# Optimization experiments

Measured on AMD Instinct MI355X. Metric: run time of the kernel, lower is better.

Reference implementation:

```python
import jax, jax.numpy as jnp
import numpy as np

B, S, HID = 1, 2048, 2048
NH = 16
QL, KVL = 1536, 512
DN, DR, DV = 128, 64, 128
DQ = DN + DR  # 192
IH, ID = 4, 128
TOPK = 1024
EPS = 1e-6
THETA = 10000.0


def rope_interleaved(x, cos, sin):
    # x: (b,s,h,d); cos/sin: (s,d//2); pairs are (x[...,2i], x[...,2i+1])
    xr = x[..., 0::2]
    xi = x[..., 1::2]
    c = cos[None, :, None, :]
    s = sin[None, :, None, :]
    yr = xr * c - xi * s
    yi = xr * s + xi * c
    return jnp.stack([yr, yi], axis=-1).reshape(x.shape)


def rope_noninterleaved(x, cos, sin):
    # rotate-half style: pairs are (x[...,i], x[...,i+d/2])
    d = x.shape[-1] // 2
    x1, x2 = x[..., :d], x[..., d:]
    c = cos[None, :, None, :]
    s = sin[None, :, None, :]
    return jnp.concatenate([x1 * c - x2 * s, x1 * s + x2 * c], axis=-1)


def rmsnorm(x, w):
    var = jnp.mean(x * x, axis=-1, keepdims=True)
    return w * (x * jax.lax.rsqrt(var + EPS))


def layernorm(x, g, b):
    mu = jnp.mean(x, axis=-1, keepdims=True)
    var = jnp.mean((x - mu) ** 2, axis=-1, keepdims=True)
    return (x - mu) * jax.lax.rsqrt(var + EPS) * g + b


def setup_inputs() -> dict:
    key = jax.random.key(0)
    ks = jax.random.split(key, 12)
    std = 0.02
    x = jax.random.normal(ks[0], (B, S, HID), jnp.float32)
    pos = jnp.arange(S, dtype=jnp.float32)
    inv_freq = THETA ** (-jnp.arange(0, DR, 2, dtype=jnp.float32) / DR)
    ang = pos[:, None] * inv_freq[None, :]  # (S, DR//2)
    cos, sin = jnp.cos(ang), jnp.sin(ang)
    mask = jnp.where(jnp.tril(jnp.ones((S, S), bool)), 0.0, -1e9).astype(jnp.float32)
    return {
        "x": x, "cos": cos, "sin": sin, "mask": mask,
        "Wq_a": jax.random.normal(ks[1], (HID, QL), jnp.float32) * std,
        "q_norm_w": jnp.ones((QL,), jnp.float32),
        "Wq_b": jax.random.normal(ks[2], (QL, NH * DQ), jnp.float32) * std,
        "Wkv_a": jax.random.normal(ks[3], (HID, KVL + DR), jnp.float32) * std,
        "kv_norm_w": jnp.ones((KVL,), jnp.float32),
        "Wkv_b": jax.random.normal(ks[4], (KVL, NH * (DN + DV)), jnp.float32) * std,
        "Wo": jax.random.normal(ks[5], (NH * DV, HID), jnp.float32) * std,
        "IWq_b": jax.random.normal(ks[6], (QL, IH * ID), jnp.float32) * std,
        "IWk": jax.random.normal(ks[7], (HID, ID), jnp.float32) * std,
        "Ik_norm_w": jnp.ones((ID,), jnp.float32),
        "Ik_norm_b": jnp.zeros((ID,), jnp.float32),
        "IWproj": jax.random.normal(ks[8], (HID, IH), jnp.float32) * std,
    }


def indexer(x, qr, cos, sin, mask, IWq_b, IWk, Ik_norm_w, Ik_norm_b, IWproj):
    b, s, _ = x.shape
    q = (qr @ IWq_b).reshape(b, s, IH, ID)
    q_pe, q_nope = q[..., :DR], q[..., DR:]
    q_pe = rope_noninterleaved(q_pe, cos, sin)
    q = jnp.concatenate([q_pe, q_nope], axis=-1)
    k = layernorm(x @ IWk, Ik_norm_w, Ik_norm_b)  # (b,s,ID)
    k_pe = rope_noninterleaved(k[:, :, None, :DR], cos, sin)[:, :, 0]
    k = jnp.concatenate([k_pe, k[..., DR:]], axis=-1)
    weights = (x @ IWproj) * (IH ** -0.5) * (ID ** -0.5)  # (b,s,IH)
    logits = jax.nn.relu(jnp.einsum('bthd,bsd->btsh', q, k))
    index_score = jnp.einsum('btsh,bth->bts', logits, weights)
    index_score = index_score + mask[None]
    k_top = min(TOPK, s)
    topk_idx = jax.lax.top_k(index_score, k_top)[1]  # (b,s,k)
    bi = jnp.arange(b)[:, None, None]
    si = jnp.arange(s)[None, :, None]
    index_mask = jnp.full((b, s, s), -1e9, jnp.float32).at[bi, si, topk_idx].set(0.0)
    return index_mask


def reference(x, cos, sin, mask, Wq_a, q_norm_w, Wq_b, Wkv_a, kv_norm_w, Wkv_b, Wo,
              IWq_b, IWk, Ik_norm_w, Ik_norm_b, IWproj):
    b, s, _ = x.shape
    qr = rmsnorm(x @ Wq_a, q_norm_w)  # (b,s,QL)
    q = (qr @ Wq_b).reshape(b, s, NH, DQ)
    q_nope, q_pe = q[..., :DN], q[..., DN:]
    q_pe = rope_interleaved(q_pe, cos, sin)
    q = jnp.concatenate([q_nope, q_pe], axis=-1)
    kv_full = x @ Wkv_a
    kv, k_pe = kv_full[..., :KVL], kv_full[..., KVL:]
    kv = rmsnorm(kv, kv_norm_w)
    k_pe = rope_interleaved(k_pe[:, :, None, :], cos, sin)  # (b,s,1,DR)
    kv_exp = (kv @ Wkv_b).reshape(b, s, NH, DN + DV)
    k_nope, v = kv_exp[..., :DN], kv_exp[..., DN:]
    k = jnp.concatenate([k_nope, jnp.broadcast_to(k_pe, (b, s, NH, DR))], axis=-1)
    scores = jnp.einsum('bshd,bthd->bsht', q, k) * (DQ ** -0.5)
    index_mask = indexer(x, qr, cos, sin, mask, IWq_b, IWk, Ik_norm_w, Ik_norm_b, IWproj)
    scores = scores + index_mask[:, :, None, :] + mask[None, :, None, :]
    probs = jax.nn.softmax(scores, axis=-1)
    out = jnp.einsum('bsht,bthd->bshd', probs, v).reshape(b, s, NH * DV)
    return out @ Wo
```

## Files before the change

kernel.cpp:

```cpp
#include <hip/hip_runtime.h>
#include <math.h>
#include <stdint.h>

#define S 2048
#define HID 2048
#define NH 16
#define QL 1536
#define KVL 512
#define DN 128
#define DR 64
#define DV 128
#define DQ 192
#define IH 4
#define ID 128
#define TOPK 1024

#define N1 2244
#define N2 3584

#define CDIV(a,b) (((a)+(b)-1)/(b))

typedef float f32x4 __attribute__((ext_vector_type(4)));
typedef short bf16x8 __attribute__((ext_vector_type(8)));

__device__ __forceinline__ ushort f2b(float f) {
    uint32_t u = __float_as_uint(f);
    u += 0x7fffu + ((u >> 16) & 1u);
    return (ushort)(u >> 16);
}

#define GLL16(g, l)                                                            \
    __builtin_amdgcn_global_load_lds(                                          \
        (const __attribute__((address_space(1))) void*)(g),                    \
        (__attribute__((address_space(3))) void*)(l), 16, 0, 0)

__global__ __launch_bounds__(256) void gemm_bt(const ushort* __restrict__ A,
                                               const ushort* __restrict__ BT,
                                               float* __restrict__ C,
                                               int M, int N, int K) {
    __shared__ ushort As[2][128 * 64];
    __shared__ ushort Bs[2][128 * 64];
    const int tid = threadIdx.x;
    const int w = tid >> 6, l = tid & 63;
    const int quad = l >> 4, lane = l & 15;
    const int row0 = blockIdx.y * 128, col0 = blockIdx.x * 128;
    const int wr = (w >> 1) * 64, wc = (w & 1) * 64;
    f32x4 acc[4][4];
#pragma unroll
    for (int i = 0; i < 4; i++)
#pragma unroll
        for (int j = 0; j < 4; j++) acc[i][j] = (f32x4)0.f;

    const int r32 = tid >> 3;
    const int csw = (((tid & 7) ^ (r32 & 7)) * 8);
    const ushort* pA[4];
    const ushort* pB[4];
#pragma unroll
    for (int p = 0; p < 4; p++) {
        pA[p] = A + (size_t)(row0 + p * 32 + r32) * K + csw;
        int bn = col0 + p * 32 + r32; if (bn > N - 1) bn = N - 1;
        pB[p] = BT + (size_t)bn * K + csw;
    }
    const int doff = r32 * 64 + (tid & 7) * 8;

#define STG64(k0, s)                                                           \
    {                                                                          \
        _Pragma("unroll")                                                      \
        for (int p = 0; p < 4; p++) {                                          \
            GLL16(pA[p] + (k0), &As[s][p * 2048 + doff]);                      \
            GLL16(pB[p] + (k0), &Bs[s][p * 2048 + doff]);                      \
        }                                                                      \
    }

    const int nt = K >> 6;
    STG64(0, 0);
    asm volatile("s_waitcnt vmcnt(0)" ::: "memory");
    __builtin_amdgcn_s_barrier();

    const int xsw = (lane & 7) << 3;
    int cur = 0;
    for (int t = 0; t < nt; ++t) {
        if (t + 1 < nt) STG64((t + 1) * 64, cur ^ 1);
#pragma unroll
        for (int kk = 0; kk < 2; kk++) {
            const int fo = (kk * 32 + quad * 8) ^ xsw;
            bf16x8 af[4], bf[4];
#pragma unroll
            for (int mi = 0; mi < 4; mi++)
                af[mi] = *(const bf16x8*)(&As[cur][(wr + mi * 16 + lane) * 64 + fo]);
#pragma unroll
            for (int ni = 0; ni < 4; ni++)
                bf[ni] = *(const bf16x8*)(&Bs[cur][(wc + ni * 16 + lane) * 64 + fo]);
#pragma unroll
            for (int mi = 0; mi < 4; mi++)
#pragma unroll
                for (int ni = 0; ni < 4; ni++)
                    acc[mi][ni] = __builtin_amdgcn_mfma_f32_16x16x32_bf16(af[mi], bf[ni], acc[mi][ni], 0, 0, 0);
        }
        asm volatile("s_waitcnt vmcnt(0)" ::: "memory");
        __builtin_amdgcn_s_barrier();
        cur ^= 1;
    }
#pragma unroll
    for (int mi = 0; mi < 4; mi++)
#pragma unroll
        for (int ni = 0; ni < 4; ni++)
#pragma unroll
            for (int r = 0; r < 4; r++) {
                int row = row0 + wr + mi * 16 + quad * 4 + r;
                int col = col0 + wc + ni * 16 + lane;
                if (col < N) C[(size_t)row * N + col] = acc[mi][ni][r];
            }
}

__global__ __launch_bounds__(256) void gemm_bt_h(const ushort* __restrict__ A,
                                                 const ushort* __restrict__ BT,
                                                 ushort* __restrict__ C,
                                                 int M, int N, int K) {
    __shared__ ushort As[2][128 * 64];
    __shared__ ushort Bs[2][128 * 64];
    const int tid = threadIdx.x;
    const int w = tid >> 6, l = tid & 63;
    const int quad = l >> 4, lane = l & 15;
    const int row0 = blockIdx.y * 128, col0 = blockIdx.x * 128;
    const int wr = (w >> 1) * 64, wc = (w & 1) * 64;
    f32x4 acc[4][4];
#pragma unroll
    for (int i = 0; i < 4; i++)
#pragma unroll
        for (int j = 0; j < 4; j++) acc[i][j] = (f32x4)0.f;

    const int r32 = tid >> 3;
    const int csw = (((tid & 7) ^ (r32 & 7)) * 8);
    const ushort* pA[4];
    const ushort* pB[4];
#pragma unroll
    for (int p = 0; p < 4; p++) {
        pA[p] = A + (size_t)(row0 + p * 32 + r32) * K + csw;
        int bn = col0 + p * 32 + r32; if (bn > N - 1) bn = N - 1;
        pB[p] = BT + (size_t)bn * K + csw;
    }
    const int doff = r32 * 64 + (tid & 7) * 8;

    const int nt = K >> 6;
    STG64(0, 0);
    asm volatile("s_waitcnt vmcnt(0)" ::: "memory");
    __builtin_amdgcn_s_barrier();

    const int xsw = (lane & 7) << 3;
    int cur = 0;
    for (int t = 0; t < nt; ++t) {
        if (t + 1 < nt) STG64((t + 1) * 64, cur ^ 1);
#pragma unroll
        for (int kk = 0; kk < 2; kk++) {
            const int fo = (kk * 32 + quad * 8) ^ xsw;
            bf16x8 af[4], bf[4];
#pragma unroll
            for (int mi = 0; mi < 4; mi++)
                af[mi] = *(const bf16x8*)(&As[cur][(wr + mi * 16 + lane) * 64 + fo]);
#pragma unroll
            for (int ni = 0; ni < 4; ni++)
                bf[ni] = *(const bf16x8*)(&Bs[cur][(wc + ni * 16 + lane) * 64 + fo]);
#pragma unroll
            for (int mi = 0; mi < 4; mi++)
#pragma unroll
                for (int ni = 0; ni < 4; ni++)
                    acc[mi][ni] = __builtin_amdgcn_mfma_f32_16x16x32_bf16(af[mi], bf[ni], acc[mi][ni], 0, 0, 0);
        }
        asm volatile("s_waitcnt vmcnt(0)" ::: "memory");
        __builtin_amdgcn_s_barrier();
        cur ^= 1;
    }
#pragma unroll
    for (int mi = 0; mi < 4; mi++)
#pragma unroll
        for (int ni = 0; ni < 4; ni++)
#pragma unroll
            for (int r = 0; r < 4; r++) {
                int row = row0 + wr + mi * 16 + quad * 4 + r;
                int col = col0 + wc + ni * 16 + lane;
                if (col < N) C[(size_t)row * N + col] = f2b(acc[mi][ni][r]);
            }
}

__device__ __forceinline__ void wtrans_body(const float* W, ushort* WT, int K, int N,
                                            int k0, int n0) {
    __shared__ float t[64][65];
    int rr = threadIdx.x >> 6, cc = threadIdx.x & 63;
#pragma unroll
    for (int p = 0; p < 16; p++) {
        int k = k0 + p * 4 + rr, n = n0 + cc;
        t[p * 4 + rr][cc] = (k < K && n < N) ? W[(size_t)k * N + n] : 0.f;
    }
    __syncthreads();
#pragma unroll
    for (int p = 0; p < 16; p++) {
        int n = n0 + p * 4 + rr, k = k0 + cc;
        if (n < N && k < K) WT[(size_t)n * K + k] = f2b(t[cc][p * 4 + rr]);
    }
}

__global__ __launch_bounds__(256) void wtrans(const float* __restrict__ W, ushort* __restrict__ WT,
                                              int K, int N) {
    wtrans_body(W, WT, K, N, blockIdx.x * 64, blockIdx.y * 64);
}

__global__ __launch_bounds__(256) void wtrans_c1(const float* __restrict__ W0, const float* __restrict__ W1,
                                                 const float* __restrict__ W2, const float* __restrict__ W3,
                                                 ushort* __restrict__ WT) {
    int yb = blockIdx.y;
    const float* W; int N; size_t off; int y;
    if (yb < 24)      { W = W0; N = 1536; off = 0;                      y = yb; }
    else if (yb < 33) { W = W1; N = 576;  off = (size_t)1536 * HID;     y = yb - 24; }
    else if (yb < 35) { W = W2; N = 128;  off = (size_t)2112 * HID;     y = yb - 33; }
    else              { W = W3; N = 4;    off = (size_t)2240 * HID;     y = yb - 35; }
    wtrans_body(W, WT + off, HID, N, blockIdx.x * 64, y * 64);
}

__global__ __launch_bounds__(256) void wtrans_c2(const float* __restrict__ W0, const float* __restrict__ W1,
                                                 ushort* __restrict__ WT) {
    int yb = blockIdx.y;
    const float* W; int N; size_t off; int y;
    if (yb < 48) { W = W0; N = 3072; off = 0;                  y = yb; }
    else         { W = W1; N = 512;  off = (size_t)3072 * QL;  y = yb - 48; }
    wtrans_body(W, WT + off, QL, N, blockIdx.x * 64, y * 64);
}

__global__ void cvt_bf16(const float* __restrict__ in, ushort* __restrict__ out) {
    int i = blockIdx.x * 256 + threadIdx.x;
    float4 v = *(const float4*)(in + (size_t)i * 4);
    uint32_t lo = (uint32_t)f2b(v.x) | ((uint32_t)f2b(v.y) << 16);
    uint32_t hi = (uint32_t)f2b(v.z) | ((uint32_t)f2b(v.w) << 16);
    *(uint2*)(out + (size_t)i * 4) = make_uint2(lo, hi);
}

__global__ __launch_bounds__(256) void post_c1(const float* __restrict__ C1,
                                               const float* __restrict__ qw,
                                               const float* __restrict__ kvw,
                                               const float* __restrict__ ikg,
                                               const float* __restrict__ ikb,
                                               const float* __restrict__ cosb,
                                               const float* __restrict__ sinb,
                                               ushort* __restrict__ qrb,
                                               ushort* __restrict__ kvnb,
                                               float* __restrict__ kpe,
                                               float* __restrict__ kiT) {
    const int t = blockIdx.x, tid = threadIdx.x;
    const float* row = C1 + (size_t)t * N1;
    __shared__ float red[256];
    __shared__ float kis[128];
    float ss = 0.f;
    for (int i = tid; i < 1536; i += 256) { float v = row[i]; ss += v * v; }
    red[tid] = ss; __syncthreads();
    for (int st = 128; st > 0; st >>= 1) { if (tid < st) red[tid] += red[tid + st]; __syncthreads(); }
    float sq = rsqrtf(red[0] / 1536.f + 1e-6f);
    __syncthreads();
    float s2 = 0.f;
    for (int i = tid; i < 512; i += 256) { float v = row[1536 + i]; s2 += v * v; }
    red[tid] = s2; __syncthreads();
    for (int st = 128; st > 0; st >>= 1) { if (tid < st) red[tid] += red[tid + st]; __syncthreads(); }
    float skv = rsqrtf(red[0] / 512.f + 1e-6f);
    __syncthreads();
    float kv_ = (tid < 128) ? row[2112 + tid] : 0.f;
    red[tid] = kv_; __syncthreads();
    for (int st = 128; st > 0; st >>= 1) { if (tid < st) red[tid] += red[tid + st]; __syncthreads(); }
    float mu = red[0] / 128.f;
    __syncthreads();
    red[tid] = kv_ * kv_; __syncthreads();
    for (int st = 128; st > 0; st >>= 1) { if (tid < st) red[tid] += red[tid + st]; __syncthreads(); }
    float var = red[0] / 128.f - mu * mu;
    for (int i = tid; i < 1536; i += 256) qrb[(size_t)t * QL + i] = f2b(row[i] * sq * qw[i]);
    for (int i = tid; i < 512; i += 256)  kvnb[(size_t)t * KVL + i] = f2b(row[1536 + i] * skv * kvw[i]);
    if (tid < 32) {
        float c = cosb[t * 32 + tid], s = sinb[t * 32 + tid];
        float xr = row[2048 + 2 * tid], xi = row[2048 + 2 * tid + 1];
        kpe[t * 64 + 2 * tid]     = xr * c - xi * s;
        kpe[t * 64 + 2 * tid + 1] = xr * s + xi * c;
    }
    if (tid < 128) kis[tid] = (kv_ - mu) * rsqrtf(var + 1e-6f) * ikg[tid] + ikb[tid];
    __syncthreads();
    if (tid < 128) {
        float outv;
        if (tid < 32) {
            float c = cosb[t * 32 + tid], s = sinb[t * 32 + tid];
            outv = kis[tid] * c - kis[tid + 32] * s;
        } else if (tid < 64) {
            int j = tid - 32;
            float c = cosb[t * 32 + j], s = sinb[t * 32 + j];
            outv = kis[j] * s + kis[tid] * c;
        } else {
            outv = kis[tid];
        }
        kiT[(size_t)tid * S + t] = outv;
    }
}

__global__ __launch_bounds__(256) void post_c2(float* __restrict__ C2,
                                               const float* __restrict__ cosb,
                                               const float* __restrict__ sinb,
                                               ushort* __restrict__ qb) {
    const int t = blockIdx.x, tid = threadIdx.x;
    __shared__ float cs[32], sn[32];
    if (tid < 32) { cs[tid] = cosb[t * 32 + tid]; sn[tid] = sinb[t * 32 + tid]; }
    __syncthreads();
    const float sc = 0.10412775370051047f;
    const float* src0 = C2 + (size_t)t * N2;
    for (int i = tid; i < NH * 96; i += 256) {
        int h = i / 96, p = i % 96;
        const float* src = src0 + h * 192;
        ushort* dst = qb + ((size_t)h * S + t) * 192;
        if (p < 64) {
            dst[2 * p]     = f2b(src[2 * p] * sc);
            dst[2 * p + 1] = f2b(src[2 * p + 1] * sc);
        } else {
            int j = p - 64;
            float c = cs[j], s = sn[j];
            float xr = src[128 + 2 * j], xi = src[128 + 2 * j + 1];
            dst[128 + 2 * j]     = f2b((xr * c - xi * s) * sc);
            dst[128 + 2 * j + 1] = f2b((xr * s + xi * c) * sc);
        }
    }
    if (tid < 128) {
        int h = tid >> 5, j = tid & 31;
        float* p = C2 + (size_t)t * N2 + 3072 + h * 128;
        float c = cs[j], s = sn[j];
        float x1 = p[j], x2 = p[j + 32];
        p[j] = x1 * c - x2 * s;
        p[j + 32] = x1 * s + x2 * c;
    }
}

__global__ __launch_bounds__(256) void pack_kv(const ushort* __restrict__ kvexp_h,
                                               const float* __restrict__ kpe,
                                               ushort* __restrict__ kb,
                                               ushort* __restrict__ vT) {
    __shared__ ushort t[64][136];
    const int s0 = blockIdx.x * 64, h = blockIdx.y, tid = threadIdx.x;
    const int row = tid >> 2, c = tid & 3;
    const ushort* src = kvexp_h + (size_t)(s0 + row) * 4096 + h * 256;
    ushort* kbr = kb + ((size_t)h * S + s0 + row) * 192;
#pragma unroll
    for (int i = 0; i < 4; i++) {
        int off = c * 32 + i * 8;
        *(uint4*)(kbr + off) = *(const uint4*)(src + off);
        *(uint4*)(&t[row][off]) = *(const uint4*)(src + 128 + off);
    }
    const float* kp = kpe + (size_t)(s0 + row) * 64 + c * 16;
#pragma unroll
    for (int i = 0; i < 16; i++) kbr[128 + c * 16 + i] = f2b(kp[i]);
    __syncthreads();
    const int d = tid >> 1, sh = (tid & 1) * 32;
    ushort* dst = vT + ((size_t)h * 128 + d) * S + s0 + sh;
#pragma unroll
    for (int i = 0; i < 32; i++) dst[i] = t[sh + i][d];
}

__global__ __launch_bounds__(256) void iscore4(const float* __restrict__ qi,
                                               const float* __restrict__ kiT,
                                               const float* __restrict__ iw,
                                               float* __restrict__ iscore) {
    int t = blockIdx.x;
    int s0 = blockIdx.y * 1024;
    if (s0 > t) return;
    int s = s0 + threadIdx.x * 4;
    __shared__ float qs[4 * ID];
    __shared__ float ws4[4];
    for (int i = threadIdx.x; i < 4 * ID; i += 256) qs[i] = qi[(size_t)t * N2 + i];
    if (threadIdx.x < 4) ws4[threadIdx.x] = iw[(size_t)t * N1 + threadIdx.x] * 0.04419417382415922f;
    __syncthreads();
    if (s > t) return;
    float a[4][4];
#pragma unroll
    for (int h = 0; h < 4; h++)
#pragma unroll
        for (int c = 0; c < 4; c++) a[h][c] = 0.f;
    for (int d = 0; d < ID; d++) {
        float4 kv = *(const float4*)(kiT + (size_t)d * S + s);
#pragma unroll
        for (int h = 0; h < 4; h++) {
            float qv = qs[h * ID + d];
            a[h][0] += qv * kv.x; a[h][1] += qv * kv.y;
            a[h][2] += qv * kv.z; a[h][3] += qv * kv.w;
        }
    }
#pragma unroll
    for (int c = 0; c < 4; c++) {
        if (s + c > t) break;
        float sc = fmaxf(a[0][c], 0.f) * ws4[0] + fmaxf(a[1][c], 0.f) * ws4[1] +
                   fmaxf(a[2][c], 0.f) * ws4[2] + fmaxf(a[3][c], 0.f) * ws4[3];
        iscore[(size_t)t * S + s + c] = sc;
    }
}

__device__ inline unsigned sortable_u32(float f) {
    unsigned u = __float_as_uint(f);
    return (u & 0x80000000u) ? ~u : (u | 0x80000000u);
}

__global__ __launch_bounds__(256) void topk_mask(const float* __restrict__ iscore,
                                                 uint32_t* __restrict__ msk) {
    int t = blockIdx.x, tid = threadIdx.x;
    uint32_t* mrow = msk + (size_t)t * 64;
    if (t < TOPK) {
        if (tid < 64) {
            int full = (t + 1) >> 5;
            uint32_t wv2 = (tid < full) ? 0xFFFFFFFFu : 0u;
            if (tid == full) { int rem = (t + 1) & 31; wv2 = rem ? ((1u << rem) - 1u) : 0u; }
            mrow[tid] = wv2;
        }
        return;
    }
    const float* row = iscore + (size_t)t * S;
    const int n = t + 1;
    const int wv = tid >> 6;
    __shared__ int hist[4][256];
    __shared__ int scan[256];
    __shared__ int bsel, ksel;
    __shared__ uint32_t bytes[256];

    int jb = tid * 8;
    float4 v0 = *(const float4*)(row + jb);
    float4 v1 = *(const float4*)(row + jb + 4);
    uint32_t lsu[8];
    {
        float vvv[8] = {v0.x, v0.y, v0.z, v0.w, v1.x, v1.y, v1.z, v1.w};
#pragma unroll
        for (int i = 0; i < 8; i++)
            lsu[i] = (jb + i < n) ? sortable_u32(vvv[i]) : 0u;
    }
    unsigned prefix = 0, prefmask = 0;
    int k = TOPK;
    for (int pass = 0; pass < 4; pass++) {
        int shift = 24 - pass * 8;
#pragma unroll
        for (int r = 0; r < 4; r++) hist[r][tid] = 0;
        __syncthreads();
#pragma unroll
        for (int i = 0; i < 8; i++) {
            uint32_t u = lsu[i];
            if ((u & prefmask) == prefix) atomicAdd(&hist[wv][(u >> shift) & 255], 1);
        }
        __syncthreads();
        int h = hist[0][tid] + hist[1][tid] + hist[2][tid] + hist[3][tid];
        scan[tid] = h; __syncthreads();
        for (int st = 1; st < 256; st <<= 1) {
            int a = scan[tid];
            int b = (tid + st < 256) ? scan[tid + st] : 0;
            __syncthreads();
            scan[tid] = a + b;
            __syncthreads();
        }
        int snext = (tid < 255) ? scan[tid + 1] : 0;
        if (scan[tid] >= k && snext < k) { bsel = tid; ksel = k - snext; }
        __syncthreads();
        prefix |= ((unsigned)bsel) << shift;
        prefmask |= 0xFFu << shift;
        k = ksel;
        __syncthreads();
    }
    const unsigned u_thr = prefix;
    const int need = k;
    uint32_t gtbits = 0, eqbits = 0;
    int eqcnt = 0;
#pragma unroll
    for (int i = 0; i < 8; i++) {
        uint32_t u = lsu[i];
        if (u > u_thr) gtbits |= 1u << i;
        else if (u == u_thr) { eqbits |= 1u << i; eqcnt++; }
    }
    scan[tid] = eqcnt; __syncthreads();
    for (int st = 1; st < 256; st <<= 1) {
        int a = scan[tid];
        int b = (tid >= st) ? scan[tid - st] : 0;
        __syncthreads();
        scan[tid] = a + b;
        __syncthreads();
    }
    int room = need - (scan[tid] - eqcnt);
    uint32_t keep = 0;
#pragma unroll
    for (int i = 0; i < 8; i++)
        if ((eqbits >> i) & 1u) { if (room > 0) { keep |= 1u << i; room--; } }
    bytes[tid] = gtbits | keep;
    __syncthreads();
    if (tid < 64)
        mrow[tid] = bytes[tid * 4] | (bytes[tid * 4 + 1] << 8) |
                    (bytes[tid * 4 + 2] << 16) | (bytes[tid * 4 + 3] << 24);
}

__global__ __launch_bounds__(256, 2) void fattn6(const ushort* __restrict__ qb,
                                                 const ushort* __restrict__ kb,
                                                 const ushort* __restrict__ vT,
                                                 const uint32_t* __restrict__ msk,
                                                 float* __restrict__ Opart,
                                                 float* __restrict__ mlbuf) {
    __shared__ ushort Ks[24 * 512];
    __shared__ ushort Vs[16 * 512];
    __shared__ ushort Pm[4][16 * 72];
    const int tid = threadIdx.x;
    const int w = tid >> 6, l = tid & 63, quad = l >> 4, lane = l & 15;
    const int b = blockIdx.x;
    const int r8 = b & 7, j = b >> 3;
    const int h = r8 + 8 * (j & 1);
    const int idx = j >> 1;
    const int pair = idx & 15, part = idx >> 4;
    const int ta = pair, tb = 31 - pair, nA = ta + 1;
    const int vlo = part * 11, vhi = vlo + 11;
    const int qa0 = ta * 64, qb0 = tb * 64;

    bf16x8 qfa[6], qfb[6];
    {
        const ushort* qpa = qb + ((size_t)h * S + qa0 + w * 16 + lane) * 192;
        const ushort* qpb = qb + ((size_t)h * S + qb0 + w * 16 + lane) * 192;
#pragma unroll
        for (int ks = 0; ks < 6; ks++) {
            qfa[ks] = *(const bf16x8*)(qpa + ks * 32 + quad * 8);
            qfb[ks] = *(const bf16x8*)(qpb + ks * 32 + quad * 8);
        }
    }
    f32x4 oa[8], ob[8];
#pragma unroll
    for (int i = 0; i < 8; i++) { oa[i] = (f32x4)0.f; ob[i] = (f32x4)0.f; }
    float ma[4], la[4], mb[4], lb[4];
#pragma unroll
    for (int r = 0; r < 4; r++) { ma[r] = -1e30f; la[r] = 0.f; mb[r] = -1e30f; lb[r] = 0.f; }

    ushort* pw = &Pm[w][0];
    const ushort* kbase = kb + (size_t)h * S * 192;
    const ushort* vbase = vT + (size_t)h * 128 * S;

    for (int kt = 0; kt <= tb; kt++) {
        const int idxB = (kt <= ta) ? 2 * kt : kt + nA;
        const int hasA = (kt <= ta);
        const int idxA = 2 * kt + 1;
        const bool doB = (idxB >= vlo && idxB < vhi);
        const bool doA = hasA && (idxA >= vlo && idxA < vhi);
        if (!(doA || doB)) continue;
        const int s0 = kt * 64;
        __syncthreads();
#pragma unroll
        for (int ii = 0; ii < 6; ii++) {
            const int i = w * 6 + ii;
            const int ks = i >> 2, kq = i & 3;
            const ushort* src = kbase + (size_t)(s0 + kq * 16 + lane) * 192 + ks * 32 + quad * 8;
            GLL16(src, Ks + i * 512 + l * 8);
        }
#pragma unroll
        for (int ii = 0; ii < 4; ii++) {
            const int i = w * 4 + ii;
            const int k2 = i >> 3, nt = i & 7;
            const ushort* src = vbase + (size_t)(nt * 16 + lane) * S + s0 + k2 * 32 + quad * 8;
            GLL16(src, Vs + i * 512 + l * 8);
        }
        __syncthreads();

#pragma unroll
        for (int pass = 0; pass < 2; pass++) {
            if (pass == 0 && !doA) continue;
            if (pass == 1 && !doB) continue;
            const bf16x8* qf = (pass == 0) ? qfa : qfb;
            f32x4* oacc      = (pass == 0) ? oa : ob;
            float* mm        = (pass == 0) ? ma : mb;
            float* ll        = (pass == 0) ? la : lb;
            const int q0t    = (pass == 0) ? qa0 : qb0;

            f32x4 sc[4];
#pragma unroll
            for (int kq = 0; kq < 4; kq++) {
                sc[kq] = (f32x4)0.f;
#pragma unroll
                for (int ks = 0; ks < 6; ks++) {
                    bf16x8 bfr = *(const bf16x8*)(Ks + (ks * 4 + kq) * 512 + quad * 128 + lane * 8);
                    sc[kq] = __builtin_amdgcn_mfma_f32_16x16x32_bf16(qf[ks], bfr, sc[kq], 0, 0, 0);
                }
            }
            uint32_t w0[4], w1[4];
            {
                const int rowbase = q0t + w * 16 + quad * 4;
#pragma unroll
                for (int r = 0; r < 4; r++) {
                    const uint32_t* mp = msk + (size_t)(rowbase + r) * 64 + (s0 >> 5);
                    w0[r] = mp[0]; w1[r] = mp[1];
                }
            }
            float vmax[4] = {-1e30f, -1e30f, -1e30f, -1e30f};
#pragma unroll
            for (int kq = 0; kq < 4; kq++) {
                const int sh = (kq & 1) * 16 + lane;
#pragma unroll
                for (int r = 0; r < 4; r++) {
                    uint32_t word = (kq < 2) ? w0[r] : w1[r];
                    float v = ((word >> sh) & 1u) ? sc[kq][r] : -1e30f;
                    sc[kq][r] = v;
                    vmax[r] = fmaxf(vmax[r], v);
                }
            }
#pragma unroll
            for (int off = 1; off < 16; off <<= 1)
#pragma unroll
                for (int r = 0; r < 4; r++)
                    vmax[r] = fmaxf(vmax[r], __shfl_xor(vmax[r], off, 64));
            float alpha[4], psum[4];
#pragma unroll
            for (int r = 0; r < 4; r++) {
                float mnew = fmaxf(mm[r], vmax[r]);
                alpha[r] = exp2f(mm[r] - mnew);
                mm[r] = mnew;
                psum[r] = 0.f;
            }
#pragma unroll
            for (int kq = 0; kq < 4; kq++)
#pragma unroll
                for (int r = 0; r < 4; r++) {
                    float v = sc[kq][r];
                    float e = (v < -1e29f) ? 0.f : exp2f(v - mm[r]);
                    psum[r] += e;
                    pw[(quad * 4 + r) * 72 + kq * 16 + lane] = f2b(e);
                }
#pragma unroll
            for (int off = 1; off < 16; off <<= 1)
#pragma unroll
                for (int r = 0; r < 4; r++)
                    psum[r] += __shfl_xor(psum[r], off, 64);
#pragma unroll
            for (int r = 0; r < 4; r++) ll[r] = ll[r] * alpha[r] + psum[r];

            bf16x8 pfr[2];
#pragma unroll
            for (int k2 = 0; k2 < 2; k2++)
                pfr[k2] = *(const bf16x8*)(pw + lane * 72 + k2 * 32 + quad * 8);
#pragma unroll
            for (int nt = 0; nt < 8; nt++) {
#pragma unroll
                for (int r = 0; r < 4; r++) oacc[nt][r] *= alpha[r];
#pragma unroll
                for (int k2 = 0; k2 < 2; k2++) {
                    bf16x8 vfr = *(const bf16x8*)(Vs + ((k2 * 8 + nt) * 4 + quad) * 128 + lane * 8);
                    oacc[nt] = __builtin_amdgcn_mfma_f32_16x16x32_bf16(pfr[k2], vfr, oacc[nt], 0, 0, 0);
                }
            }
        }
    }
#pragma unroll
    for (int pass = 0; pass < 2; pass++) {
        const f32x4* oacc = (pass == 0) ? oa : ob;
        const float* mm   = (pass == 0) ? ma : mb;
        const float* ll   = (pass == 0) ? la : lb;
        const int qt      = (pass == 0) ? ta : tb;
        float* Op = Opart + (size_t)((qt * 16 + h) * 3 + part) * (64 * 128);
        float* mlp = mlbuf + (size_t)((qt * 16 + h) * 3 + part) * 128;
#pragma unroll
        for (int nt = 0; nt < 8; nt++)
#pragma unroll
            for (int r = 0; r < 4; r++)
                Op[(w * 16 + quad * 4 + r) * 128 + nt * 16 + lane] = oacc[nt][r];
        if (lane == 0) {
#pragma unroll
            for (int r = 0; r < 4; r++) {
                mlp[(w * 16 + quad * 4 + r) * 2 + 0] = mm[r];
                mlp[(w * 16 + quad * 4 + r) * 2 + 1] = ll[r];
            }
        }
    }
}

__global__ __launch_bounds__(256) void attn_combine(const float* __restrict__ Opart,
                                                    const float* __restrict__ mlbuf,
                                                    ushort* __restrict__ attn_b) {
    const int qt = blockIdx.x, h = blockIdx.y, tid = threadIdx.x;
    const size_t base = ((size_t)qt * 16 + h) * 3;
    const float* Op0 = Opart + base * 8192;
    const float* Op1 = Op0 + 8192;
    const float* Op2 = Op1 + 8192;
    const float* ml0 = mlbuf + base * 128;
    const float* ml1 = ml0 + 128;
    const float* ml2 = ml1 + 128;
#pragma unroll
    for (int i = 0; i < 32; i++) {
        int id = tid + i * 256;
        int row = id >> 7, d = id & 127;
        float m0 = ml0[row * 2], l0 = ml0[row * 2 + 1];
        float m1 = ml1[row * 2], l1 = ml1[row * 2 + 1];
        float m2 = ml2[row * 2], l2 = ml2[row * 2 + 1];
        float m = fmaxf(fmaxf(m0, m1), m2);
        float e0 = exp2f(m0 - m), e1 = exp2f(m1 - m), e2 = exp2f(m2 - m);
        float linv = 1.f / (l0 * e0 + l1 * e1 + l2 * e2);
        float v = (Op0[id] * e0 + Op1[id] * e1 + Op2[id] * e2) * linv;
        attn_b[(size_t)(qt * 64 + row) * 2048 + h * 128 + d] = f2b(v);
    }
}

extern "C" void kernel_launch(void* const* d_in, const int* in_sizes, int n_in,
                              void* d_out, int out_size, void* d_ws, size_t ws_size,
                              hipStream_t stream) {
    const float* x        = (const float*)d_in[0];
    const float* cosb     = (const float*)d_in[1];
    const float* sinb     = (const float*)d_in[2];
    const float* Wq_a     = (const float*)d_in[4];
    const float* q_norm_w = (const float*)d_in[5];
    const float* Wq_b     = (const float*)d_in[6];
    const float* Wkv_a    = (const float*)d_in[7];
    const float* kv_norm_w= (const float*)d_in[8];
    const float* Wkv_b    = (const float*)d_in[9];
    const float* Wo       = (const float*)d_in[10];
    const float* IWq_b    = (const float*)d_in[11];
    const float* IWk      = (const float*)d_in[12];
    const float* Ik_norm_w= (const float*)d_in[13];
    const float* Ik_norm_b= (const float*)d_in[14];
    const float* IWproj   = (const float*)d_in[15];
    float* out = (float*)d_out;

    char* ws = (char*)d_ws;
    size_t o = 0;
    auto take = [&](size_t b) { char* p = ws + o; o += (b + 255) & ~(size_t)255; return p; };
    ushort* xb     = (ushort*)take((size_t)S * HID * 2);
    ushort* qrb    = (ushort*)take((size_t)S * QL * 2);
    ushort* qb     = (ushort*)take((size_t)NH * S * DQ * 2);
    ushort* kvnb   = (ushort*)take((size_t)S * KVL * 2);
    float*  kpe    = (float*)take((size_t)S * DR * 4);
    ushort* kb     = (ushort*)take((size_t)NH * S * DQ * 2);
    ushort* vT     = (ushort*)take((size_t)NH * DV * S * 2);
    uint32_t* msk  = (uint32_t*)take((size_t)S * 64 * 4);
    float*  mlbuf  = (float*)take((size_t)32 * 16 * 3 * 64 * 2 * 4);
    ushort* WTp    = (ushort*)take((size_t)N2 * QL * 2);
    float*  C1     = (float*)take((size_t)S * N1 * 4);
    char*   big    = take((size_t)32 * 16 * 3 * 8192 * 4 + 1024);
    ushort* kvexp_h= (ushort*)take((size_t)S * 4096 * 2);
    float*  kiT    = (float*)take((size_t)128 * S * 4);
    char*   poolb  = take((size_t)16777216);

    float* C2     = (float*)big;
    float* Opart  = (float*)big;
    float* iscore = (float*)poolb;
    ushort* attn_b = (ushort*)poolb;

    cvt_bf16<<<(S * HID) / 1024, 256, 0, stream>>>(x, xb);

    wtrans_c1<<<dim3(32, 36), 256, 0, stream>>>(Wq_a, Wkv_a, IWk, IWproj, WTp);
    gemm_bt<<<dim3(CDIV(N1, 128), S / 128), 256, 0, stream>>>(xb, WTp, C1, S, N1, HID);
    post_c1<<<S, 256, 0, stream>>>(C1, q_norm_w, kv_norm_w, Ik_norm_w, Ik_norm_b,
                                   cosb, sinb, qrb, kvnb, kpe, kiT);

    wtrans_c2<<<dim3(24, 56), 256, 0, stream>>>(Wq_b, IWq_b, WTp);
    gemm_bt<<<dim3(N2 / 128, S / 128), 256, 0, stream>>>(qrb, WTp, C2, S, N2, QL);
    post_c2<<<S, 256, 0, stream>>>(C2, cosb, sinb, qb);

    wtrans<<<dim3(8, 64), 256, 0, stream>>>(Wkv_b, WTp, KVL, NH * (DN + DV));
    gemm_bt_h<<<dim3(32, S / 128), 256, 0, stream>>>(kvnb, WTp, kvexp_h, S, NH * (DN + DV), KVL);
    pack_kv<<<dim3(S / 64, NH), 256, 0, stream>>>(kvexp_h, kpe, kb, vT);

    iscore4<<<dim3(S, S / 1024), 256, 0, stream>>>(C2 + 3072, kiT, C1 + 2240, iscore);
    topk_mask<<<S, 256, 0, stream>>>(iscore, msk);

    fattn6<<<768, 256, 0, stream>>>(qb, kb, vT, msk, Opart, mlbuf);
    attn_combine<<<dim3(32, 16), 256, 0, stream>>>(Opart, mlbuf, attn_b);

    wtrans<<<dim3(32, 32), 256, 0, stream>>>(Wo, WTp, NH * DV, HID);
    gemm_bt<<<dim3(HID / 128, S / 128), 256, 0, stream>>>(attn_b, WTp, out, S, HID, NH * DV);

    (void)in_sizes; (void)n_in; (void)out_size; (void)ws_size; (void)o;
}
```

Baseline: 496.6 us.

## Register-block indexer scores over four queries and use wave-shuffle scans in top-k

```diff
diff --git a/kernel.cpp b/kernel.cpp
--- a/kernel.cpp
+++ b/kernel.cpp
@@ -355,40 +355,61 @@
     for (int i = 0; i < 32; i++) dst[i] = t[sh + i][d];
 }
 
-__global__ __launch_bounds__(256) void iscore4(const float* __restrict__ qi,
-                                               const float* __restrict__ kiT,
-                                               const float* __restrict__ iw,
-                                               float* __restrict__ iscore) {
-    int t = blockIdx.x;
-    int s0 = blockIdx.y * 1024;
-    if (s0 > t) return;
-    int s = s0 + threadIdx.x * 4;
-    __shared__ float qs[4 * ID];
-    __shared__ float ws4[4];
-    for (int i = threadIdx.x; i < 4 * ID; i += 256) qs[i] = qi[(size_t)t * N2 + i];
-    if (threadIdx.x < 4) ws4[threadIdx.x] = iw[(size_t)t * N1 + threadIdx.x] * 0.04419417382415922f;
-    __syncthreads();
-    if (s > t) return;
-    float a[4][4];
-#pragma unroll
-    for (int h = 0; h < 4; h++)
-#pragma unroll
-        for (int c = 0; c < 4; c++) a[h][c] = 0.f;
+__global__ __launch_bounds__(256) void iscore4x4(const float* __restrict__ qi,
+                                                 const float* __restrict__ kiT,
+                                                 const float* __restrict__ iw,
+                                                 float* __restrict__ iscore) {
+    const int t0 = blockIdx.x * 4;
+    const int s0 = blockIdx.y * 1024;
+    if (s0 > t0 + 3) return;
+    const int s = s0 + threadIdx.x * 4;
+    __shared__ float qsT[4 * ID * 4];
+    __shared__ float ws[16];
+    for (int i = threadIdx.x; i < 4 * ID * 4; i += 256) {
+        int tt = i & 3, hd = i >> 2;
+        qsT[hd * 4 + tt] = qi[(size_t)(t0 + tt) * N2 + hd];
+    }
+    if (threadIdx.x < 16) {
+        int tt = threadIdx.x >> 2, h = threadIdx.x & 3;
+        ws[threadIdx.x] = iw[(size_t)(t0 + tt) * N1 + h] * 0.04419417382415922f;
+    }
+    __syncthreads();
+    if (s > t0 + 3) return;
+    float a[4][4][4];
+#pragma unroll
+    for (int tt = 0; tt < 4; tt++)
+#pragma unroll
+        for (int h = 0; h < 4; h++)
+#pragma unroll
+            for (int c = 0; c < 4; c++) a[tt][h][c] = 0.f;
     for (int d = 0; d < ID; d++) {
         float4 kv = *(const float4*)(kiT + (size_t)d * S + s);
 #pragma unroll
         for (int h = 0; h < 4; h++) {
-            float qv = qs[h * ID + d];
-            a[h][0] += qv * kv.x; a[h][1] += qv * kv.y;
-            a[h][2] += qv * kv.z; a[h][3] += qv * kv.w;
-        }
-    }
-#pragma unroll
-    for (int c = 0; c < 4; c++) {
-        if (s + c > t) break;
-        float sc = fmaxf(a[0][c], 0.f) * ws4[0] + fmaxf(a[1][c], 0.f) * ws4[1] +
-                   fmaxf(a[2][c], 0.f) * ws4[2] + fmaxf(a[3][c], 0.f) * ws4[3];
-        iscore[(size_t)t * S + s + c] = sc;
+            float4 qv = *(const float4*)(&qsT[(h * ID + d) * 4]);
+            a[0][h][0] += qv.x * kv.x; a[0][h][1] += qv.x * kv.y;
+            a[0][h][2] += qv.x * kv.z; a[0][h][3] += qv.x * kv.w;
+            a[1][h][0] += qv.y * kv.x; a[1][h][1] += qv.y * kv.y;
+            a[1][h][2] += qv.y * kv.z; a[1][h][3] += qv.y * kv.w;
+            a[2][h][0] += qv.z * kv.x; a[2][h][1] += qv.z * kv.y;
+            a[2][h][2] += qv.z * kv.z; a[2][h][3] += qv.z * kv.w;
+            a[3][h][0] += qv.w * kv.x; a[3][h][1] += qv.w * kv.y;
+            a[3][h][2] += qv.w * kv.z; a[3][h][3] += qv.w * kv.w;
+        }
+    }
+#pragma unroll
+    for (int tt = 0; tt < 4; tt++) {
+        const int t = t0 + tt;
+        if (s > t) continue;
+#pragma unroll
+        for (int c = 0; c < 4; c++) {
+            if (s + c > t) break;
+            float sc = fmaxf(a[tt][0][c], 0.f) * ws[tt * 4 + 0] +
+                       fmaxf(a[tt][1][c], 0.f) * ws[tt * 4 + 1] +
+                       fmaxf(a[tt][2][c], 0.f) * ws[tt * 4 + 2] +
+                       fmaxf(a[tt][3][c], 0.f) * ws[tt * 4 + 3];
+            iscore[(size_t)t * S + s + c] = sc;
+        }
     }
 }
 
@@ -412,9 +433,9 @@
     }
     const float* row = iscore + (size_t)t * S;
     const int n = t + 1;
-    const int wv = tid >> 6;
+    const int wv = tid >> 6, lane = tid & 63;
     __shared__ int hist[4][256];
-    __shared__ int scan[256];
+    __shared__ int wtot[4];
     __shared__ int bsel, ksel;
     __shared__ uint32_t bytes[256];
 
@@ -442,16 +463,20 @@
         }
         __syncthreads();
         int h = hist[0][tid] + hist[1][tid] + hist[2][tid] + hist[3][tid];
-        scan[tid] = h; __syncthreads();
-        for (int st = 1; st < 256; st <<= 1) {
-            int a = scan[tid];
-            int b = (tid + st < 256) ? scan[tid + st] : 0;
-            __syncthreads();
-            scan[tid] = a + b;
-            __syncthreads();
-        }
-        int snext = (tid < 255) ? scan[tid + 1] : 0;
-        if (scan[tid] >= k && snext < k) { bsel = tid; ksel = k - snext; }
+        int x = h;
+#pragma unroll
+        for (int off = 1; off < 64; off <<= 1) {
+            int tmp = __shfl_down(x, off, 64);
+            if (lane + off < 64) x += tmp;
+        }
+        if (lane == 0) wtot[wv] = x;
+        __syncthreads();
+        int add = 0;
+#pragma unroll
+        for (int w2 = 1; w2 < 4; w2++) if (w2 > wv) add += wtot[w2];
+        x += add;
+        int snext = x - h;
+        if (x >= k && snext < k) { bsel = tid; ksel = k - snext; }
         __syncthreads();
         prefix |= ((unsigned)bsel) << shift;
         prefmask |= 0xFFu << shift;
@@ -468,20 +493,26 @@
         if (u > u_thr) gtbits |= 1u << i;
         else if (u == u_thr) { eqbits |= 1u << i; eqcnt++; }
     }
-    scan[tid] = eqcnt; __syncthreads();
-    for (int st = 1; st < 256; st <<= 1) {
-        int a = scan[tid];
-        int b = (tid >= st) ? scan[tid - st] : 0;
+    {
+        int x = eqcnt;
+#pragma unroll
+        for (int off = 1; off < 64; off <<= 1) {
+            int tmp = __shfl_up(x, off, 64);
+            if (lane >= off) x += tmp;
+        }
+        if (lane == 63) wtot[wv] = x;
         __syncthreads();
-        scan[tid] = a + b;
-        __syncthreads();
-    }
-    int room = need - (scan[tid] - eqcnt);
-    uint32_t keep = 0;
-#pragma unroll
-    for (int i = 0; i < 8; i++)
-        if ((eqbits >> i) & 1u) { if (room > 0) { keep |= 1u << i; room--; } }
-    bytes[tid] = gtbits | keep;
+        int add = 0;
+#pragma unroll
+        for (int w2 = 0; w2 < 3; w2++) if (w2 < wv) add += wtot[w2];
+        x += add;
+        int room = need - (x - eqcnt);
+        uint32_t keep = 0;
+#pragma unroll
+        for (int i = 0; i < 8; i++)
+            if ((eqbits >> i) & 1u) { if (room > 0) { keep |= 1u << i; room--; } }
+        bytes[tid] = gtbits | keep;
+    }
     __syncthreads();
     if (tid < 64)
         mrow[tid] = bytes[tid * 4] | (bytes[tid * 4 + 1] << 8) |
@@ -749,7 +780,7 @@
     gemm_bt_h<<<dim3(32, S / 128), 256, 0, stream>>>(kvnb, WTp, kvexp_h, S, NH * (DN + DV), KVL);
     pack_kv<<<dim3(S / 64, NH), 256, 0, stream>>>(kvexp_h, kpe, kb, vT);
 
-    iscore4<<<dim3(S, S / 1024), 256, 0, stream>>>(C2 + 3072, kiT, C1 + 2240, iscore);
+    iscore4x4<<<dim3(S / 4, S / 1024), 256, 0, stream>>>(C2 + 3072, kiT, C1 + 2240, iscore);
     topk_mask<<<S, 256, 0, stream>>>(iscore, msk);
 
     fattn6<<<768, 256, 0, stream>>>(qb, kb, vT, msk, Opart, mlbuf);
```

New measurement: 498.3 us. About the same (+0.3%).
